# Kernel tuning notes

Measured on AMD Instinct MI355X. Metric: run time of the kernel, lower is better.

## Reference

```python
import jax, jax.numpy as jnp
import numpy as np

B, S, D = 16, 1024, 1024   # batch, n_assets, d_model
H, DK = 16, 64             # num_heads, key_dim (H*DK == D)


def setup_inputs() -> dict:
    key = jax.random.key(0)
    ks = jax.random.split(key, 6)
    scale = 0.02
    return {
        "inputs": jax.random.normal(ks[0], (B, S, D), dtype=jnp.float32),
        "lead_lag_bias": jax.random.normal(ks[1], (S, S), dtype=jnp.float32),
        "Wq": jax.random.normal(ks[2], (D, H * DK), dtype=jnp.float32) * scale,
        "Wk": jax.random.normal(ks[3], (D, H * DK), dtype=jnp.float32) * scale,
        "Wv": jax.random.normal(ks[4], (D, H * DK), dtype=jnp.float32) * scale,
        "Wo": jax.random.normal(ks[5], (H * DK, D), dtype=jnp.float32) * scale,
        "bias_transform": jnp.ones((H,), dtype=jnp.float32),
    }


def reference(inputs, lead_lag_bias, Wq, Wk, Wv, Wo, bias_transform):
    # inputs: [B, S, D]; lead_lag_bias: [S, S]
    inv_sqrt_dk = 1.0 / np.sqrt(DK)
    q = (inputs @ Wq).reshape(B, S, H, DK).transpose(0, 2, 1, 3)  # [B,H,S,Dk]
    k = (inputs @ Wk).reshape(B, S, H, DK).transpose(0, 2, 1, 3)
    v = (inputs @ Wv).reshape(B, S, H, DK).transpose(0, 2, 1, 3)
    scores = jnp.einsum('bhqd,bhkd->bhqk', q, k) * inv_sqrt_dk  # [B,H,S,S]
    # per-head scaled static lead-lag bias (broadcast over batch)
    scores = scores + bias_transform[None, :, None, None] * lead_lag_bias[None, None, :, :]
    attn = jax.nn.softmax(scores, axis=-1)
    out = jnp.einsum('bhqk,bhkd->bhqd', attn, v)  # [B,H,S,Dk]
    out = out.transpose(0, 2, 1, 3).reshape(B, S, H * DK)
    return out @ Wo  # [B, S, D]
```

## Files before the change

### kernel.cpp

```cpp
#include <hip/hip_runtime.h>

typedef __attribute__((ext_vector_type(4))) float f32x4;
typedef __attribute__((ext_vector_type(8))) __bf16 bf16x8;
typedef __attribute__((ext_vector_type(8))) unsigned short u16x8;
typedef __attribute__((ext_vector_type(2))) unsigned int u32x2;

#define MFMA16(a, b, c) \
  __builtin_amdgcn_mfma_f32_16x16x32_bf16(__builtin_bit_cast(bf16x8, (a)), \
                                          __builtin_bit_cast(bf16x8, (b)), (c), 0, 0, 0)

__device__ __forceinline__ unsigned short f2bf(float f) {
  unsigned int u = __builtin_bit_cast(unsigned int, f);
  u += 0x7FFFu + ((u >> 16) & 1u);
  return (unsigned short)(u >> 16);
}

__device__ __forceinline__ unsigned int packbf(float lo, float hi) {
  return (unsigned int)f2bf(lo) | ((unsigned int)f2bf(hi) << 16);
}

__global__ __launch_bounds__(256) void wtrans(
    const float* __restrict__ Wq, const float* __restrict__ Wk,
    const float* __restrict__ Wv, const float* __restrict__ Wo,
    unsigned short* __restrict__ Wt)
{
  __shared__ unsigned short tile[32][33];
  const int z = blockIdx.z;
  const float* W = (z == 0) ? Wq : (z == 1) ? Wk : (z == 2) ? Wv : Wo;
  unsigned short* T = Wt + (size_t)z * 1024 * 1024;
  const int tx = threadIdx.x, ty = threadIdx.y;
  const int x = blockIdx.x * 32 + tx;
  const int y0 = blockIdx.y * 32;
#pragma unroll
  for (int i = 0; i < 4; ++i)
    tile[ty + i * 8][tx] = f2bf(W[(size_t)(y0 + ty + i * 8) * 1024 + x]);
  __syncthreads();
#pragma unroll
  for (int i = 0; i < 4; ++i)
    T[(size_t)(blockIdx.x * 32 + ty + i * 8) * 1024 + y0 + tx] = tile[tx][ty + i * 8];
}

__global__ __launch_bounds__(256) void qkv_gemm(
    const float* __restrict__ X, const unsigned short* __restrict__ Wt,
    unsigned short* __restrict__ Qo, unsigned short* __restrict__ Ko,
    unsigned short* __restrict__ Vo)
{
  const int bn = blockIdx.x * 128;
  const int bm = blockIdx.y * 128;
  const int z = blockIdx.z;
  const unsigned short* Wz = Wt + (size_t)z * 1024 * 1024;
  unsigned short* Out = (z == 0) ? Qo : (z == 1) ? Ko : Vo;

  const int tid = threadIdx.x;
  const int w = tid >> 6, l = tid & 63, l15 = l & 15, lg = l >> 4;
  const int wr = w >> 1, wc = w & 1;

  __shared__ alignas(16) unsigned short sA[128][32];
  __shared__ alignas(16) unsigned short sB[128][32];

  f32x4 acc[4][4];
  const f32x4 zero = {0.f, 0.f, 0.f, 0.f};
#pragma unroll
  for (int i = 0; i < 4; ++i)
#pragma unroll
    for (int j = 0; j < 4; ++j) acc[i][j] = zero;

  for (int k0 = 0; k0 < 1024; k0 += 32) {
    __syncthreads();
#pragma unroll
    for (int p = 0; p < 2; ++p) {
      int id = p * 256 + tid;
      int row = id >> 2, c = id & 3;
      const float* src = X + (size_t)(bm + row) * 1024 + k0 + c * 8;
      f32x4 f0 = *(const f32x4*)(src);
      f32x4 f1 = *(const f32x4*)(src + 4);
      u16x8 v;
      v[0] = f2bf(f0[0]); v[1] = f2bf(f0[1]); v[2] = f2bf(f0[2]); v[3] = f2bf(f0[3]);
      v[4] = f2bf(f1[0]); v[5] = f2bf(f1[1]); v[6] = f2bf(f1[2]); v[7] = f2bf(f1[3]);
      *(u16x8*)&sA[row][c * 8] = v;
    }
#pragma unroll
    for (int p = 0; p < 2; ++p) {
      int id = p * 256 + tid;
      int row = id >> 2, c = id & 3;
      *(u16x8*)&sB[row][c * 8] =
          *(const u16x8*)(Wz + (size_t)(bn + row) * 1024 + k0 + c * 8);
    }
    __syncthreads();

    u16x8 af[4], bf[4];
#pragma unroll
    for (int m = 0; m < 4; ++m)
      af[m] = *(const u16x8*)&sA[wr * 64 + m * 16 + l15][lg * 8];
#pragma unroll
    for (int n = 0; n < 4; ++n)
      bf[n] = *(const u16x8*)&sB[wc * 64 + n * 16 + l15][lg * 8];
#pragma unroll
    for (int m = 0; m < 4; ++m)
#pragma unroll
      for (int n = 0; n < 4; ++n)
        acc[m][n] = MFMA16(af[m], bf[n], acc[m][n]);
  }

#pragma unroll
  for (int m = 0; m < 4; ++m) {
    int grow_b = bm + wr * 64 + m * 16 + lg * 4;
#pragma unroll
    for (int n = 0; n < 4; ++n) {
      int gcol = bn + wc * 64 + n * 16 + l15;
      int hh = gcol >> 6, dk = gcol & 63;
#pragma unroll
      for (int t = 0; t < 4; ++t) {
        int grow = grow_b + t;
        int bb = grow >> 10, s = grow & 1023;
        Out[(((size_t)(bb * 16 + hh)) * 1024 + s) * 64 + dk] = f2bf(acc[m][n][t]);
      }
    }
  }
}

__global__ __launch_bounds__(256) void vtrans(
    const unsigned short* __restrict__ V, unsigned short* __restrict__ Vt)
{
  __shared__ unsigned short tile[64 * 64];
  const int s0 = blockIdx.x * 64;
  const size_t bh = (size_t)blockIdx.y * (64 * 1024);
  const int tid = threadIdx.x;

#pragma unroll
  for (int p = 0; p < 2; ++p) {
    int id = p * 256 + tid;
    int s = id >> 3, cc = id & 7;
    u16x8 v = *(const u16x8*)(V + bh + (size_t)(s0 + s) * 64 + cc * 8);
    *(u16x8*)&tile[s * 64 + ((cc ^ (s >> 3)) * 8)] = v;
  }
  __syncthreads();
#pragma unroll
  for (int p = 0; p < 2; ++p) {
    int id = p * 256 + tid;
    int d = id >> 3, sc = id & 7;
    u16x8 v;
#pragma unroll
    for (int i = 0; i < 8; ++i)
      v[i] = tile[(sc * 8 + i) * 64 + (((d >> 3) ^ sc) * 8) + (d & 7)];
    *(u16x8*)(Vt + bh + (size_t)d * 1024 + s0 + sc * 8) = v;
  }
}

__global__ __launch_bounds__(256) void attn(
    const unsigned short* __restrict__ Q, const unsigned short* __restrict__ Kg,
    const unsigned short* __restrict__ Vtg, const float* __restrict__ LL,
    const float* __restrict__ btr, unsigned short* __restrict__ O)
{
  const int q0 = blockIdx.x * 64;
  const int h = blockIdx.y, b = blockIdx.z;
  const int tid = threadIdx.x;
  const int w = tid >> 6, l = tid & 63, l15 = l & 15, lg = l >> 4;

  __shared__ alignas(16) unsigned short sK[64 * 64];
  __shared__ alignas(16) unsigned short sVt[64 * 64];
  __shared__ alignas(16) unsigned short sP[4][16 * 64];

  const float bt = btr[h];
  const size_t bh = (size_t)(b * 16 + h) * (1024 * 64);
  const unsigned short* Qb = Q + bh;
  const unsigned short* Kp = Kg + bh;
  const unsigned short* Vp = Vtg + bh;

  u16x8 qf[2];
  {
    const unsigned short* qp = Qb + (size_t)(q0 + w * 16 + l15) * 64 + lg * 8;
    qf[0] = *(const u16x8*)qp;
    qf[1] = *(const u16x8*)(qp + 32);
  }
  const int qrow = q0 + w * 16 + l15;

  float mrow = -1e30f, lrow = 0.f;
  f32x4 o[4];
  const f32x4 zero = {0.f, 0.f, 0.f, 0.f};
#pragma unroll
  for (int dn = 0; dn < 4; ++dn) o[dn] = zero;

  const int srow0 = tid >> 3, scc = tid & 7;

  for (int kt = 0; kt < 16; ++kt) {
    __syncthreads();
#pragma unroll
    for (int p = 0; p < 2; ++p) {
      int row = p * 32 + srow0;
      u16x8 vk = *(const u16x8*)(Kp + (size_t)(kt * 64 + row) * 64 + scc * 8);
      u16x8 vv = *(const u16x8*)(Vp + (size_t)row * 1024 + kt * 64 + scc * 8);
      *(u16x8*)&sK[row * 64 + ((scc ^ (row & 7)) * 8)] = vk;
      *(u16x8*)&sVt[row * 64 + ((scc ^ (row & 7)) * 8)] = vv;
    }
    __syncthreads();

    f32x4 llv[4];
#pragma unroll
    for (int jn = 0; jn < 4; ++jn)
      llv[jn] = *(const f32x4*)(LL + (size_t)qrow * 1024 + kt * 64 + jn * 16 + lg * 4);

    f32x4 s[4];
#pragma unroll
    for (int jn = 0; jn < 4; ++jn) s[jn] = zero;
#pragma unroll
    for (int dc = 0; dc < 2; ++dc) {
#pragma unroll
      for (int jn = 0; jn < 4; ++jn) {
        int row = jn * 16 + l15;
        u16x8 kfr = *(const u16x8*)&sK[row * 64 + (((dc * 4 + lg) ^ (row & 7)) * 8)];
        s[jn] = MFMA16(kfr, qf[dc], s[jn]);
      }
    }

#pragma unroll
    for (int jn = 0; jn < 4; ++jn)
#pragma unroll
      for (int t = 0; t < 4; ++t)
        s[jn][t] = s[jn][t] * 0.125f + bt * llv[jn][t];

    float tm = s[0][0];
#pragma unroll
    for (int jn = 0; jn < 4; ++jn)
#pragma unroll
      for (int t = 0; t < 4; ++t) tm = fmaxf(tm, s[jn][t]);
    tm = fmaxf(tm, __shfl_xor(tm, 16, 64));
    tm = fmaxf(tm, __shfl_xor(tm, 32, 64));
    float mn = fmaxf(mrow, tm);
    float sc = __expf(mrow - mn);
    mrow = mn;

    float rs = 0.f;
    unsigned int pk[4][2];
#pragma unroll
    for (int jn = 0; jn < 4; ++jn) {
      float p0 = __expf(s[jn][0] - mn);
      float p1 = __expf(s[jn][1] - mn);
      float p2 = __expf(s[jn][2] - mn);
      float p3 = __expf(s[jn][3] - mn);
      rs += (p0 + p1) + (p2 + p3);
      pk[jn][0] = packbf(p0, p1);
      pk[jn][1] = packbf(p2, p3);
    }
    rs += __shfl_xor(rs, 16, 64);
    rs += __shfl_xor(rs, 32, 64);
    lrow = lrow * sc + rs;
#pragma unroll
    for (int dn = 0; dn < 4; ++dn) o[dn] *= sc;

#pragma unroll
    for (int jn = 0; jn < 4; ++jn) {
      int elem = l15 * 64 + (((jn * 2 + (lg >> 1)) ^ (l15 & 7)) * 8) + (lg & 1) * 4;
      u32x2 v2; v2[0] = pk[jn][0]; v2[1] = pk[jn][1];
      *(u32x2*)&sP[w][elem] = v2;
    }

#pragma unroll
    for (int kc = 0; kc < 2; ++kc) {
      u16x8 pb = *(const u16x8*)&sP[w][l15 * 64 + (((kc * 4 + lg) ^ (l15 & 7)) * 8)];
#pragma unroll
      for (int dn = 0; dn < 4; ++dn) {
        int vr = dn * 16 + l15;
        u16x8 vfr = *(const u16x8*)&sVt[vr * 64 + (((kc * 4 + lg) ^ (vr & 7)) * 8)];
        o[dn] = MFMA16(vfr, pb, o[dn]);
      }
    }
  }

  float inv = 1.f / lrow;
  unsigned short* Op = O + ((size_t)(b * 1024 + qrow)) * 1024 + h * 64;
#pragma unroll
  for (int dn = 0; dn < 4; ++dn) {
    u32x2 v2;
    v2[0] = packbf(o[dn][0] * inv, o[dn][1] * inv);
    v2[1] = packbf(o[dn][2] * inv, o[dn][3] * inv);
    *(u32x2*)(Op + dn * 16 + lg * 4) = v2;
  }
}

__global__ __launch_bounds__(256) void out_gemm(
    const unsigned short* __restrict__ A, const unsigned short* __restrict__ Bt,
    float* __restrict__ C)
{
  const int bn = blockIdx.x * 128;
  const int bm = blockIdx.y * 128;
  const int tid = threadIdx.x;
  const int w = tid >> 6, l = tid & 63, l15 = l & 15, lg = l >> 4;
  const int wr = w >> 1, wc = w & 1;

  __shared__ alignas(16) unsigned short sA[128][32];
  __shared__ alignas(16) unsigned short sB[128][32];

  f32x4 acc[4][4];
  const f32x4 zero = {0.f, 0.f, 0.f, 0.f};
#pragma unroll
  for (int i = 0; i < 4; ++i)
#pragma unroll
    for (int j = 0; j < 4; ++j) acc[i][j] = zero;

  for (int k0 = 0; k0 < 1024; k0 += 32) {
    __syncthreads();
#pragma unroll
    for (int p = 0; p < 2; ++p) {
      int id = p * 256 + tid;
      int row = id >> 2, c = id & 3;
      *(u16x8*)&sA[row][c * 8] =
          *(const u16x8*)(A + (size_t)(bm + row) * 1024 + k0 + c * 8);
      *(u16x8*)&sB[row][c * 8] =
          *(const u16x8*)(Bt + (size_t)(bn + row) * 1024 + k0 + c * 8);
    }
    __syncthreads();

    u16x8 af[4], bf[4];
#pragma unroll
    for (int m = 0; m < 4; ++m)
      af[m] = *(const u16x8*)&sA[wr * 64 + m * 16 + l15][lg * 8];
#pragma unroll
    for (int n = 0; n < 4; ++n)
      bf[n] = *(const u16x8*)&sB[wc * 64 + n * 16 + l15][lg * 8];
#pragma unroll
    for (int m = 0; m < 4; ++m)
#pragma unroll
      for (int n = 0; n < 4; ++n)
        acc[m][n] = MFMA16(af[m], bf[n], acc[m][n]);
  }

#pragma unroll
  for (int m = 0; m < 4; ++m) {
    int grow_b = bm + wr * 64 + m * 16 + lg * 4;
#pragma unroll
    for (int n = 0; n < 4; ++n) {
      int gcol = bn + wc * 64 + n * 16 + l15;
#pragma unroll
      for (int t = 0; t < 4; ++t)
        C[(size_t)(grow_b + t) * 1024 + gcol] = acc[m][n][t];
    }
  }
}

extern "C" void kernel_launch(void* const* d_in, const int* in_sizes, int n_in,
                              void* d_out, int out_size, void* d_ws, size_t ws_size,
                              hipStream_t stream) {
  const float* X  = (const float*)d_in[0];
  const float* LL = (const float*)d_in[1];
  const float* Wq = (const float*)d_in[2];
  const float* Wk = (const float*)d_in[3];
  const float* Wv = (const float*)d_in[4];
  const float* Wo = (const float*)d_in[5];
  const float* bt = (const float*)d_in[6];
  float* out = (float*)d_out;

  unsigned short* ws = (unsigned short*)d_ws;
  const size_t QKV = (size_t)16 * 16 * 1024 * 64;
  unsigned short* Qb = ws;
  unsigned short* Kb = Qb + QKV;
  unsigned short* Vb = Kb + QKV;
  unsigned short* Vt = Vb + QKV;
  unsigned short* Wt = Vt + QKV;
  unsigned short* Ob = Vb;

  wtrans<<<dim3(32, 32, 4), dim3(32, 8), 0, stream>>>(Wq, Wk, Wv, Wo, Wt);
  qkv_gemm<<<dim3(8, 128, 3), 256, 0, stream>>>(X, Wt, Qb, Kb, Vb);
  vtrans<<<dim3(16, 256), 256, 0, stream>>>(Vb, Vt);
  attn<<<dim3(16, 16, 16), 256, 0, stream>>>(Qb, Kb, Vt, LL, bt, Ob);
  out_gemm<<<dim3(8, 128), 256, 0, stream>>>(Ob, Wt + 3 * 1024 * 1024, out);
}
```

Baseline: 599.5 us.

## Pre-convert X to bf16 and stage GEMM tiles via direct global-to-LDS loads

Adds a separate kernel that converts the fp32 input to bf16 once, so the QKV GEMM no longer converts X per tile. That conversion was repeated for each of the 24 column blocks reading the same rows. Both GEMMs now fill shared memory with global_load_lds (direct global-to-LDS) instead of staging through registers. The QKV grid is flattened so blocks with the same row tile are adjacent, which should improve L2 reuse of X. The cost is an extra kernel launch plus a bf16 copy of X written into the Vt workspace, which vtrans later overwrites.

```diff
diff --git a/kernel.cpp b/kernel.cpp
--- a/kernel.cpp
+++ b/kernel.cpp
@@ -17,6 +17,24 @@
 
 __device__ __forceinline__ unsigned int packbf(float lo, float hi) {
   return (unsigned int)f2bf(lo) | ((unsigned int)f2bf(hi) << 16);
+}
+
+__device__ __forceinline__ void gload16(const void* g, void* l) {
+  __builtin_amdgcn_global_load_lds(
+      (const __attribute__((address_space(1))) void*)g,
+      (__attribute__((address_space(3))) void*)l, 16, 0, 0);
+}
+
+__global__ __launch_bounds__(256) void xconv(
+    const float* __restrict__ X, unsigned short* __restrict__ Xb)
+{
+  size_t i = ((size_t)blockIdx.x * 256 + threadIdx.x) * 8;
+  f32x4 f0 = *(const f32x4*)(X + i);
+  f32x4 f1 = *(const f32x4*)(X + i + 4);
+  u16x8 v;
+  v[0] = f2bf(f0[0]); v[1] = f2bf(f0[1]); v[2] = f2bf(f0[2]); v[3] = f2bf(f0[3]);
+  v[4] = f2bf(f1[0]); v[5] = f2bf(f1[1]); v[6] = f2bf(f1[2]); v[7] = f2bf(f1[3]);
+  *(u16x8*)(Xb + i) = v;
 }
 
 __global__ __launch_bounds__(256) void wtrans(
@@ -41,13 +59,14 @@
 }
 
 __global__ __launch_bounds__(256) void qkv_gemm(
-    const float* __restrict__ X, const unsigned short* __restrict__ Wt,
+    const unsigned short* __restrict__ Xb, const unsigned short* __restrict__ Wt,
     unsigned short* __restrict__ Qo, unsigned short* __restrict__ Ko,
     unsigned short* __restrict__ Vo)
 {
-  const int bn = blockIdx.x * 128;
+  const int bx = blockIdx.x;
+  const int z = bx >> 3;
+  const int bn = (bx & 7) * 128;
   const int bm = blockIdx.y * 128;
-  const int z = blockIdx.z;
   const unsigned short* Wz = Wt + (size_t)z * 1024 * 1024;
   unsigned short* Out = (z == 0) ? Qo : (z == 1) ? Ko : Vo;
 
@@ -58,6 +77,13 @@
   __shared__ alignas(16) unsigned short sA[128][32];
   __shared__ alignas(16) unsigned short sB[128][32];
 
+  const int srow = w * 32 + (l >> 2);
+  const int scol = (l & 3) * 8;
+  const unsigned short* gA = Xb + (size_t)(bm + srow) * 1024 + scol;
+  const unsigned short* gB = Wz + (size_t)(bn + srow) * 1024 + scol;
+  unsigned short* lA = &sA[srow][scol];
+  unsigned short* lB = &sB[srow][scol];
+
   f32x4 acc[4][4];
   const f32x4 zero = {0.f, 0.f, 0.f, 0.f};
 #pragma unroll
@@ -69,22 +95,8 @@
     __syncthreads();
 #pragma unroll
     for (int p = 0; p < 2; ++p) {
-      int id = p * 256 + tid;
-      int row = id >> 2, c = id & 3;
-      const float* src = X + (size_t)(bm + row) * 1024 + k0 + c * 8;
-      f32x4 f0 = *(const f32x4*)(src);
-      f32x4 f1 = *(const f32x4*)(src + 4);
-      u16x8 v;
-      v[0] = f2bf(f0[0]); v[1] = f2bf(f0[1]); v[2] = f2bf(f0[2]); v[3] = f2bf(f0[3]);
-      v[4] = f2bf(f1[0]); v[5] = f2bf(f1[1]); v[6] = f2bf(f1[2]); v[7] = f2bf(f1[3]);
-      *(u16x8*)&sA[row][c * 8] = v;
-    }
-#pragma unroll
-    for (int p = 0; p < 2; ++p) {
-      int id = p * 256 + tid;
-      int row = id >> 2, c = id & 3;
-      *(u16x8*)&sB[row][c * 8] =
-          *(const u16x8*)(Wz + (size_t)(bn + row) * 1024 + k0 + c * 8);
+      gload16(gA + (size_t)p * 16 * 1024 + k0, lA + p * 16 * 32);
+      gload16(gB + (size_t)p * 16 * 1024 + k0, lB + p * 16 * 32);
     }
     __syncthreads();
 
@@ -291,6 +303,13 @@
   __shared__ alignas(16) unsigned short sA[128][32];
   __shared__ alignas(16) unsigned short sB[128][32];
 
+  const int srow = w * 32 + (l >> 2);
+  const int scol = (l & 3) * 8;
+  const unsigned short* gA = A + (size_t)(bm + srow) * 1024 + scol;
+  const unsigned short* gB = Bt + (size_t)(bn + srow) * 1024 + scol;
+  unsigned short* lA = &sA[srow][scol];
+  unsigned short* lB = &sB[srow][scol];
+
   f32x4 acc[4][4];
   const f32x4 zero = {0.f, 0.f, 0.f, 0.f};
 #pragma unroll
@@ -302,12 +321,8 @@
     __syncthreads();
 #pragma unroll
     for (int p = 0; p < 2; ++p) {
-      int id = p * 256 + tid;
-      int row = id >> 2, c = id & 3;
-      *(u16x8*)&sA[row][c * 8] =
-          *(const u16x8*)(A + (size_t)(bm + row) * 1024 + k0 + c * 8);
-      *(u16x8*)&sB[row][c * 8] =
-          *(const u16x8*)(Bt + (size_t)(bn + row) * 1024 + k0 + c * 8);
+      gload16(gA + (size_t)p * 16 * 1024 + k0, lA + p * 16 * 32);
+      gload16(gB + (size_t)p * 16 * 1024 + k0, lB + p * 16 * 32);
     }
     __syncthreads();
 
@@ -358,9 +373,11 @@
   unsigned short* Vt = Vb + QKV;
   unsigned short* Wt = Vt + QKV;
   unsigned short* Ob = Vb;
-
+  unsigned short* Xbb = Vt;
+
+  xconv<<<dim3(8192), 256, 0, stream>>>(X, Xbb);
   wtrans<<<dim3(32, 32, 4), dim3(32, 8), 0, stream>>>(Wq, Wk, Wv, Wo, Wt);
-  qkv_gemm<<<dim3(8, 128, 3), 256, 0, stream>>>(X, Wt, Qb, Kb, Vb);
+  qkv_gemm<<<dim3(24, 128), 256, 0, stream>>>(Xbb, Wt, Qb, Kb, Vb);
   vtrans<<<dim3(16, 256), 256, 0, stream>>>(Vb, Vt);
   attn<<<dim3(16, 16, 16), 256, 0, stream>>>(Qb, Kb, Vt, LL, bt, Ob);
   out_gemm<<<dim3(8, 128), 256, 0, stream>>>(Ob, Wt + 3 * 1024 * 1024, out);
```

Measured after the change: 506.5 us. -15.5%, faster.
